# Performance work log

Hardware: AMD Instinct MI355X
Metric: run time of the kernel (lower is better)

Reference implementation:

```python
import jax, jax.numpy as jnp
import numpy as np

N, E, B = 20000, 320000, 16
DIN, HID, HEADS, ZDIM = 128, 128, 4, 128
NEG_SLOPE = 0.2


def _glorot(key, shape):
    fan = sum(shape[-2:]) if len(shape) >= 2 else shape[-1] * 2
    return jax.random.normal(key, shape, jnp.float32) * jnp.sqrt(2.0 / fan)


def setup_inputs() -> dict:
    key = jax.random.key(0)
    ks = jax.random.split(key, 20)
    inp = {
        "x": jax.random.normal(ks[0], (N, DIN), jnp.float32),
        "edge_index": jax.random.randint(ks[1], (2, E), 0, N),
        "batch_id": jnp.sort(jax.random.randint(ks[2], (N,), 0, B)),
        "node_mask": jax.random.bernoulli(ks[3], 0.1, (N,)),
        "edge_mask": jax.random.bernoulli(ks[4], 0.5, (E,)),
    }
    # layer dims: e_Fs=[128,128,128,128]; heads=4 on layers 0,1; heads=1 last
    dims = [(DIN, HID, HEADS), (HID * HEADS, HID, HEADS), (HID * HEADS, ZDIM, 1)]
    for li, (fin, fout, h) in enumerate(dims, start=1):
        inp[f"W{li}"] = _glorot(ks[4 + 3 * li], (fin, h * fout))
        inp[f"att_src{li}"] = _glorot(ks[5 + 3 * li], (h, fout))
        inp[f"att_dst{li}"] = _glorot(ks[6 + 3 * li], (h, fout))
        inp[f"bias{li}"] = jnp.zeros((h * fout,), jnp.float32)
    return inp


def _gat_layer(x, W, a_src, a_dst, bias, src, dst, heads, fout):
    n = x.shape[0]
    h = (x @ W).reshape(n, heads, fout)            # [N,H,F]
    alpha_s = (h * a_src).sum(-1)                  # [N,H]
    alpha_d = (h * a_dst).sum(-1)                  # [N,H]
    e = jax.nn.leaky_relu(alpha_s[src] + alpha_d[dst], NEG_SLOPE)  # [E,H]
    m = jax.ops.segment_max(e, dst, num_segments=n)
    ex = jnp.exp(e - m[dst])
    denom = jax.ops.segment_sum(ex, dst, num_segments=n)
    w = ex / denom[dst]                            # segment softmax over incoming edges
    out = jax.ops.segment_sum(h[src] * w[:, :, None], dst, num_segments=n)  # [N,H,F]
    return out.reshape(n, heads * fout) + bias


def reference(x, edge_index, batch_id, node_mask, edge_mask,
              W1, att_src1, att_dst1, bias1,
              W2, att_src2, att_dst2, bias2,
              W3, att_src3, att_dst3, bias3):
    n = x.shape[0]
    loop = jnp.arange(n)
    src = jnp.concatenate([edge_index[0], loop])   # add_self_loops=True
    dst = jnp.concatenate([edge_index[1], loop])
    # edge_mask is passed as edge_attr but GATConv has edge_dim=None -> ignored
    h = _gat_layer(x, W1, att_src1, att_dst1, bias1, src, dst, HEADS, HID)
    h = jax.nn.relu(h)
    h = _gat_layer(h, W2, att_src2, att_dst2, bias2, src, dst, HEADS, HID)
    h = jax.nn.relu(h)
    h = _gat_layer(h, W3, att_src3, att_dst3, bias3, src, dst, 1, ZDIM)
    # masked global max pool: if mask.sum()>0 pool over ~mask else all nodes
    has_masked = jnp.any(node_mask)
    valid = jnp.logical_or(~node_mask, ~has_masked)
    neg = jnp.asarray(-1e30, h.dtype)
    vals = jnp.where(valid[:, None], h, neg)
    return jax.ops.segment_max(vals, batch_id, num_segments=B)
```

## Files before the change

### kernel.cpp

```cpp
#include <hip/hip_runtime.h>
#include <stdint.h>


#define NN 20000
#define MPAD 20480
#define NE 320000
#define NBATCH 16
#define NEG 0.2f
#define WSCALE 64.0f
#define WINV 0.015625f

using f16x8 = __attribute__((ext_vector_type(8))) _Float16;
using f32x4 = __attribute__((ext_vector_type(4))) float;
using h2 = __attribute__((ext_vector_type(2))) _Float16;

#define GLL16(gp, lp)                                                        \
  __builtin_amdgcn_global_load_lds(                                          \
      (const __attribute__((address_space(1))) void*)(gp),                   \
      (__attribute__((address_space(3))) void*)(lp), 16, 0, 0)

static __device__ __forceinline__ unsigned short h2u(_Float16 h) {
  union { _Float16 f; unsigned short u; } c;
  c.f = h;
  return c.u;
}
static __device__ __forceinline__ float u2f(unsigned short u) {
  union { unsigned short u; _Float16 f; } c;
  c.u = u;
  return (float)c.f;
}
static __device__ __forceinline__ h2 bits2h2(unsigned v) {
  union { unsigned u; h2 h; } c;
  c.u = v;
  return c.h;
}
static __device__ __forceinline__ unsigned h22bits(h2 h) {
  union { h2 h; unsigned u; } c;
  c.h = h;
  return c.u;
}
static __device__ __forceinline__ unsigned encf(float f) {
  unsigned u = __float_as_uint(f);
  return (u & 0x80000000u) ? ~u : (u | 0x80000000u);
}
static __device__ __forceinline__ float decf(unsigned u) {
  return __uint_as_float((u & 0x80000000u) ? (u ^ 0x80000000u) : ~u);
}

#define R1 (512 * 128)
#define R2 (512 * 512)
#define R3 (128 * 512)
#define PREPTOT (R1 + R2 + R3 + NN * 128)
__global__ void k_init_prep(const float* __restrict__ W1, const float* __restrict__ W2,
                            const float* __restrict__ W3, const float* __restrict__ x,
                            unsigned short* __restrict__ wt1,
                            unsigned short* __restrict__ wt2,
                            unsigned short* __restrict__ wt3,
                            unsigned short* __restrict__ xp, int* deg,
                            unsigned* enc, int* flag, float* alz, int alcount) {
  int idx = blockIdx.x * blockDim.x + threadIdx.x;
  if (idx < R1) {
    int n = idx & 511, k = idx >> 9;
    wt1[(size_t)n * 128 + k] = h2u((_Float16)(W1[(size_t)k * 512 + n] * WSCALE));
  } else if (idx < R1 + R2) {
    int j = idx - R1;
    int n = j & 511, k = j >> 9;
    wt2[(size_t)n * 512 + k] = h2u((_Float16)(W2[(size_t)k * 512 + n] * WSCALE));
  } else if (idx < R1 + R2 + R3) {
    int j = idx - (R1 + R2);
    int n = j & 127, k = j >> 7;
    wt3[(size_t)n * 512 + k] = h2u((_Float16)(W3[(size_t)k * 128 + n] * WSCALE));
  } else if (idx < PREPTOT) {
    int j = idx - (R1 + R2 + R3);
    xp[j] = h2u((_Float16)x[j]);
  }
  if (idx < NN) deg[idx] = 1;
  if (idx < NBATCH * 128) enc[idx] = ~__float_as_uint(-1e30f);
  if (idx == 0) *flag = 0;
  if (idx < alcount) alz[idx] = 0.f;
}

__global__ void k_count(const int* __restrict__ ei, int* __restrict__ deg) {
  int e = blockIdx.x * blockDim.x + threadIdx.x;
  if (e < NE) atomicAdd(&deg[ei[NE + e]], 1);
}

__global__ void k_scan(const int* __restrict__ deg, int* __restrict__ row_ptr,
                       int* __restrict__ cursor) {
  __shared__ int wsum[16];
  int t = threadIdx.x;
  int lane = t & 63, wid = t >> 6;
  const int CH = 20;
  int beg = t * CH;
  int s = 0;
  for (int i = 0; i < CH; i++) {
    int idx = beg + i;
    if (idx < NN) s += deg[idx];
  }
  int incl = s;
  for (int off = 1; off < 64; off <<= 1) {
    int v = __shfl_up(incl, off, 64);
    if (lane >= off) incl += v;
  }
  if (lane == 63) wsum[wid] = incl;
  __syncthreads();
  if (t < 16) {
    int v = wsum[t];
    int in2 = v;
    for (int off = 1; off < 16; off <<= 1) {
      int u = __shfl_up(in2, off, 16);
      if (t >= off) in2 += u;
    }
    wsum[t] = in2 - v;
  }
  __syncthreads();
  int run = wsum[wid] + incl - s;
  for (int i = 0; i < CH; i++) {
    int idx = beg + i;
    if (idx < NN) {
      row_ptr[idx] = run;
      cursor[idx] = run;
      run += deg[idx];
    }
  }
  if (t == 1023) row_ptr[NN] = run;
}

__global__ void k_fill(const int* __restrict__ ei, int* __restrict__ cursor,
                       int* __restrict__ col, const int* __restrict__ nmask,
                       int* __restrict__ flag) {
  int i = blockIdx.x * blockDim.x + threadIdx.x;
  if (i >= NE + NN) return;
  int src, dst;
  if (i < NE) {
    src = ei[i];
    dst = ei[NE + i];
  } else {
    src = dst = i - NE;
    if (nmask[src] != 0) *flag = 1;
  }
  int pos = atomicAdd(&cursor[dst], 1);
  col[pos] = src;
}

#define BN 128
#define BK 32

template <int BMT, int NT, bool SWIZ>
__global__ __launch_bounds__(NT, 4) void k_gemm(
    const unsigned short* __restrict__ Ap, const unsigned short* __restrict__ Wt,
    unsigned short* __restrict__ C, const float* __restrict__ attS,
    const float* __restrict__ attD, float* __restrict__ alS,
    float* __restrict__ alD, int K, int Nc, int H) {
  __shared__ __align__(16) unsigned short As[BMT][BK];
  __shared__ __align__(16) unsigned short Bs[BN][BK];
  int tid = threadIdx.x;
  int bm, bn;
  if constexpr (SWIZ) {
    int id = blockIdx.x;
    int r = id & 7, t = id >> 3;
    bn = (t & 3) * BN;
    bm = (((t >> 2) << 3) + r) * BMT;
  } else {
    bm = blockIdx.y * BMT;
    bn = blockIdx.x * BN;
  }
  int wid = tid >> 6, lane = tid & 63;
  int wm = (BMT == 128) ? (wid >> 1) * 64 : 0;
  int wn = (BMT == 128) ? (wid & 1) * 64 : wid * 64;
  int lrow = lane & 15, lquad = lane >> 4;

  f32x4 acc[4][4] = {};

  for (int k0 = 0; k0 < K; k0 += BK) {
    __syncthreads();
#pragma unroll
    for (int i = 0; i < (BMT * 4) / NT; i++) {
      int slot = tid + NT * i;
      int row = slot >> 2;
      int ks = (slot & 3) * 8;
      GLL16(Ap + (size_t)(bm + row) * K + k0 + ks, &As[0][0] + (size_t)slot * 8);
    }
#pragma unroll
    for (int i = 0; i < 512 / NT; i++) {
      int slot = tid + NT * i;
      int row = slot >> 2;
      int ks = (slot & 3) * 8;
      GLL16(Wt + (size_t)(bn + row) * K + k0 + ks, &Bs[0][0] + (size_t)slot * 8);
    }
    __syncthreads();

    f16x8 af[4];
#pragma unroll
    for (int mf = 0; mf < 4; mf++)
      af[mf] = *(const f16x8*)&As[wm + mf * 16 + lrow][lquad * 8];
#pragma unroll
    for (int nf = 0; nf < 4; nf++) {
      f16x8 bf = *(const f16x8*)&Bs[wn + nf * 16 + lrow][lquad * 8];
#pragma unroll
      for (int mf = 0; mf < 4; mf++)
        acc[mf][nf] =
            __builtin_amdgcn_mfma_f32_16x16x32_f16(bf, af[mf], acc[mf][nf], 0, 0, 0);
    }
  }
#pragma unroll
  for (int mf = 0; mf < 4; mf++)
#pragma unroll
    for (int nf = 0; nf < 4; nf++)
#pragma unroll
      for (int r = 0; r < 4; r++) acc[mf][nf][r] *= WINV;

  float4 aS[4], aD[4];
#pragma unroll
  for (int nf = 0; nf < 4; nf++) {
    int n0 = bn + wn + nf * 16 + lquad * 4;
    aS[nf] = *(const float4*)(attS + n0);
    aD[nf] = *(const float4*)(attD + n0);
  }
  int head = bn >> 7;
#pragma unroll
  for (int mf = 0; mf < 4; mf++) {
    float ps = 0.f, pd = 0.f;
#pragma unroll
    for (int nf = 0; nf < 4; nf++) {
      ps += acc[mf][nf][0] * aS[nf].x + acc[mf][nf][1] * aS[nf].y +
            acc[mf][nf][2] * aS[nf].z + acc[mf][nf][3] * aS[nf].w;
      pd += acc[mf][nf][0] * aD[nf].x + acc[mf][nf][1] * aD[nf].y +
            acc[mf][nf][2] * aD[nf].z + acc[mf][nf][3] * aD[nf].w;
    }
    ps += __shfl_xor(ps, 16, 64);
    ps += __shfl_xor(ps, 32, 64);
    pd += __shfl_xor(pd, 16, 64);
    pd += __shfl_xor(pd, 32, 64);
    int row = bm + wm + mf * 16 + lrow;
    if (lquad == 0) {
      atomicAdd(&alS[(size_t)row * H + head], ps);
      atomicAdd(&alD[(size_t)row * H + head], pd);
    }
  }
#pragma unroll
  for (int mf = 0; mf < 4; mf++) {
    int m = bm + wm + mf * 16 + lrow;
#pragma unroll
    for (int nf = 0; nf < 4; nf++) {
      int n0 = bn + wn + nf * 16 + lquad * 4;
      ushort4 o;
      o.x = h2u((_Float16)acc[mf][nf][0]);
      o.y = h2u((_Float16)acc[mf][nf][1]);
      o.z = h2u((_Float16)acc[mf][nf][2]);
      o.w = h2u((_Float16)acc[mf][nf][3]);
      *(ushort4*)(C + (size_t)m * Nc + n0) = o;
    }
  }
}

template <int HF, int NG>
static __device__ __forceinline__ void gat_gather(
    const unsigned long long* __restrict__ cwp, int je, int se,
    const unsigned short* __restrict__ hb, h2& ha0, h2& ha1, h2& ha2, h2& ha3) {
  unsigned long long q[NG];
  uint4 v[NG];
#pragma unroll
  for (int r = 0; r < NG; r++) q[r] = cwp[je + se + 4 * r];
#pragma unroll
  for (int r = 0; r < NG; r++)
    v[r] = *(const uint4*)(hb + (size_t)(unsigned)q[r] * HF);
#pragma unroll
  for (int r = 0; r < NG; r++) {
    h2 hw = bits2h2((unsigned)(q[r] >> 32));
    ha0 += hw * bits2h2(v[r].x);
    ha1 += hw * bits2h2(v[r].y);
    ha2 += hw * bits2h2(v[r].z);
    ha3 += hw * bits2h2(v[r].w);
  }
}

template <int H, bool RELU, bool FP16OUT, bool PIN>
__global__ __launch_bounds__(256) void k_agg(
    const unsigned short* __restrict__ h, const float* __restrict__ as_,
    const float* __restrict__ ad_, const int* __restrict__ row_ptr,
    const int* __restrict__ col, const float* __restrict__ bias,
    float* __restrict__ out, unsigned short* __restrict__ outp) {
  constexpr int HF = H * 128;
  __shared__ unsigned long long cw[4][64];
  int tid = threadIdx.x, bwid = tid >> 6, lane = tid & 63;
  int node, sub;
  if constexpr (PIN) {
    sub = blockIdx.x & 3;
    node = (blockIdx.x >> 2) * 4 + bwid;
  } else {
    node = blockIdx.x * 4 + bwid;
    sub = 0;
    if (node >= NN) return;
  }
  int beg = row_ptr[node], end = row_ptr[node + 1];
  int deg = end - beg;
  float adv = ad_[(size_t)node * H + sub];
  float shift = (adv > 0.f) ? adv : NEG * adv;
  float fscale = 1.f;
  bool fast = (deg <= 64);

  if (__builtin_expect(fast, 1)) {
    unsigned sidx = 0;
    float t = 0.f;
    if (lane < deg) {
      sidx = (unsigned)col[beg + lane];
      float e = as_[(size_t)sidx * H + sub] + adv;
      e = (e > 0.f) ? e : NEG * e;
      t = fminf(__expf(e - shift), 60000.f);
    }
    _Float16 ht = (_Float16)t;
    h2 hv;
    hv[0] = ht;
    hv[1] = ht;
    cw[bwid][lane] = ((unsigned long long)h22bits(hv) << 32) | sidx;
    float S = t;
#pragma unroll
    for (int off = 32; off; off >>= 1) S += __shfl_xor(S, off, 64);
    fscale = 1.f / S;
  }
  float Mr = 0.f, Sinv = 0.f;
  if (!fast) {
    float m = -1e30f, s = 0.f;
    for (int j = beg + lane; j < end; j += 64) {
      int sidx = col[j];
      float e = as_[(size_t)sidx * H + sub] + adv;
      e = (e > 0.f) ? e : NEG * e;
      float nm = fmaxf(m, e);
      s = s * __expf(m - nm) + __expf(e - nm);
      m = nm;
    }
    float mm = m;
#pragma unroll
    for (int off = 32; off; off >>= 1) mm = fmaxf(mm, __shfl_xor(mm, off, 64));
    float t = s * __expf(m - mm);
#pragma unroll
    for (int off = 32; off; off >>= 1) t += __shfl_xor(t, off, 64);
    Mr = mm;
    Sinv = 1.f / t;
  }

  const int se = lane >> 4;
  const int fb = sub * 128 + (lane & 15) * 8;
  const unsigned short* __restrict__ hb = h + fb;
  float facc[8] = {0.f, 0.f, 0.f, 0.f, 0.f, 0.f, 0.f, 0.f};
  for (int c0 = beg; c0 < end; c0 += 64) {
    int cnt = min(64, end - c0);
    if (!fast) {
      unsigned sidx = 0;
      float w = 0.f;
      if (lane < cnt) {
        sidx = (unsigned)col[c0 + lane];
        float e = as_[(size_t)sidx * H + sub] + adv;
        e = (e > 0.f) ? e : NEG * e;
        w = __expf(e - Mr) * Sinv;
      }
      _Float16 hw = (_Float16)w;
      h2 hv;
      hv[0] = hw;
      hv[1] = hw;
      cw[bwid][lane] = ((unsigned long long)h22bits(hv) << 32) | sidx;
    }
    h2 ha0 = {(_Float16)0.f, (_Float16)0.f};
    h2 ha1 = ha0, ha2 = ha0, ha3 = ha0;
    int je = 0;
    while (je < cnt) {
      if (cnt - je > 16) {
        gat_gather<HF, 8>(cw[bwid], je, se, hb, ha0, ha1, ha2, ha3);
        je += 32;
      } else {
        gat_gather<HF, 4>(cw[bwid], je, se, hb, ha0, ha1, ha2, ha3);
        je += 16;
      }
    }
    facc[0] += (float)ha0[0];
    facc[1] += (float)ha0[1];
    facc[2] += (float)ha1[0];
    facc[3] += (float)ha1[1];
    facc[4] += (float)ha2[0];
    facc[5] += (float)ha2[1];
    facc[6] += (float)ha3[0];
    facc[7] += (float)ha3[1];
  }
#pragma unroll
  for (int k = 0; k < 8; k++) {
    facc[k] += __shfl_xor(facc[k], 16, 64);
    facc[k] += __shfl_xor(facc[k], 32, 64);
  }
  if (lane < 16) {
    float4 b0 = *(const float4*)(bias + fb);
    float4 b1 = *(const float4*)(bias + fb + 4);
    float v0 = facc[0] * fscale + b0.x, v1 = facc[1] * fscale + b0.y;
    float v2 = facc[2] * fscale + b0.z, v3 = facc[3] * fscale + b0.w;
    float v4 = facc[4] * fscale + b1.x, v5 = facc[5] * fscale + b1.y;
    float v6 = facc[6] * fscale + b1.z, v7 = facc[7] * fscale + b1.w;
    if (RELU) {
      v0 = fmaxf(v0, 0.f);
      v1 = fmaxf(v1, 0.f);
      v2 = fmaxf(v2, 0.f);
      v3 = fmaxf(v3, 0.f);
      v4 = fmaxf(v4, 0.f);
      v5 = fmaxf(v5, 0.f);
      v6 = fmaxf(v6, 0.f);
      v7 = fmaxf(v7, 0.f);
    }
    if constexpr (FP16OUT) {
      h2 p0, p1, p2, p3;
      p0[0] = (_Float16)v0;
      p0[1] = (_Float16)v1;
      p1[0] = (_Float16)v2;
      p1[1] = (_Float16)v3;
      p2[0] = (_Float16)v4;
      p2[1] = (_Float16)v5;
      p3[0] = (_Float16)v6;
      p3[1] = (_Float16)v7;
      uint4 o;
      o.x = h22bits(p0);
      o.y = h22bits(p1);
      o.z = h22bits(p2);
      o.w = h22bits(p3);
      *(uint4*)(outp + (size_t)node * HF + fb) = o;
    } else {
      *(float4*)(out + (size_t)node * HF + fb) = make_float4(v0, v1, v2, v3);
      *(float4*)(out + (size_t)node * HF + fb + 4) = make_float4(v4, v5, v6, v7);
    }
  }
}

__global__ void k_pool(const unsigned short* __restrict__ h,
                       const int* __restrict__ batch,
                       const int* __restrict__ mask, const int* __restrict__ flag,
                       unsigned* __restrict__ enc) {
  int f = threadIdx.x;
  int n0 = blockIdx.x * 32;
  if (n0 >= NN) return;
  int n1 = min(NN, n0 + 32);
  int any = *flag;
  float local = -1e30f;
  int curb = batch[n0];
  for (int n = n0; n < n1; ++n) {
    int b = batch[n];
    if (b != curb) {
      if (local > -1e30f) atomicMax(&enc[curb * 128 + f], encf(local));
      local = -1e30f;
      curb = b;
    }
    bool valid = (mask[n] == 0) || (!any);
    if (valid) local = fmaxf(local, u2f(h[(size_t)n * 128 + f]));
  }
  if (local > -1e30f) atomicMax(&enc[curb * 128 + f], encf(local));
}

__global__ void k_out(const unsigned* __restrict__ enc, float* __restrict__ out) {
  int i = blockIdx.x * blockDim.x + threadIdx.x;
  if (i < NBATCH * 128) out[i] = decf(enc[i]);
}

extern "C" void kernel_launch(void* const* d_in, const int* in_sizes, int n_in,
                              void* d_out, int out_size, void* d_ws, size_t ws_size,
                              hipStream_t stream) {
  const float* x = (const float*)d_in[0];
  const int* ei = (const int*)d_in[1];
  const int* batch = (const int*)d_in[2];
  const int* nmask = (const int*)d_in[3];
  const float* W1 = (const float*)d_in[5];
  const float* as1 = (const float*)d_in[6];
  const float* ad1 = (const float*)d_in[7];
  const float* b1 = (const float*)d_in[8];
  const float* W2 = (const float*)d_in[9];
  const float* as2 = (const float*)d_in[10];
  const float* ad2 = (const float*)d_in[11];
  const float* b2 = (const float*)d_in[12];
  const float* W3 = (const float*)d_in[13];
  const float* as3 = (const float*)d_in[14];
  const float* ad3 = (const float*)d_in[15];
  const float* b3 = (const float*)d_in[16];

  char* ws = (char*)d_ws;
  size_t off = 0;
  auto alloc = [&](size_t bytes) -> char* {
    char* p = ws + off;
    off = (off + bytes + 255) & ~(size_t)255;
    return p;
  };
  unsigned short* hA = (unsigned short*)alloc((size_t)MPAD * 512 * 2);
  unsigned short* hG = (unsigned short*)alloc((size_t)MPAD * 512 * 2);
  float* out3 = (float*)alloc((size_t)MPAD * 128 * 4);
  unsigned short* xP = (unsigned short*)out3;
  unsigned short* out3h = (unsigned short*)out3;
  unsigned short* wt1 = (unsigned short*)alloc((size_t)512 * 128 * 2);
  unsigned short* wt2 = (unsigned short*)alloc((size_t)512 * 512 * 2);
  unsigned short* wt3 = (unsigned short*)alloc((size_t)128 * 512 * 2);
  char* alStart = ws + off;
  float* alS1 = (float*)alloc((size_t)MPAD * 4 * 4);
  float* alD1 = (float*)alloc((size_t)MPAD * 4 * 4);
  float* alS2 = (float*)alloc((size_t)MPAD * 4 * 4);
  float* alD2 = (float*)alloc((size_t)MPAD * 4 * 4);
  float* alS3 = (float*)alloc((size_t)MPAD * 4);
  float* alD3 = (float*)alloc((size_t)MPAD * 4);
  int alcount = (int)(((ws + off) - alStart) / 4);
  int* deg = (int*)alloc((size_t)NN * 4);
  int* cursor = (int*)alloc((size_t)NN * 4);
  int* rowp = (int*)alloc((size_t)(NN + 1) * 4);
  int* colx = (int*)alloc((size_t)(NE + NN) * 4);
  unsigned* enc = (unsigned*)alloc((size_t)NBATCH * 128 * 4);
  int* flag = (int*)alloc(4);
  (void)ws_size; (void)n_in; (void)in_sizes; (void)out_size;

  k_init_prep<<<(PREPTOT + 255) / 256, 256, 0, stream>>>(
      W1, W2, W3, x, wt1, wt2, wt3, xP, deg, enc, flag, (float*)alStart, alcount);
  k_count<<<(NE + 255) / 256, 256, 0, stream>>>(ei, deg);
  k_scan<<<1, 1024, 0, stream>>>(deg, rowp, cursor);
  k_fill<<<(NE + NN + 255) / 256, 256, 0, stream>>>(ei, cursor, colx, nmask, flag);

  const int gemmBlocks = 4 * (MPAD / 128);
  dim3 gg3(1, MPAD / 64);

  k_gemm<128, 256, true><<<gemmBlocks, 256, 0, stream>>>(
      xP, wt1, hA, as1, ad1, alS1, alD1, 128, 512, 4);
  k_agg<4, true, true, true><<<NN, 256, 0, stream>>>(hA, alS1, alD1, rowp, colx,
                                                     b1, nullptr, hG);
  k_gemm<128, 256, true><<<gemmBlocks, 256, 0, stream>>>(
      hG, wt2, hA, as2, ad2, alS2, alD2, 512, 512, 4);
  k_agg<4, true, true, true><<<NN, 256, 0, stream>>>(hA, alS2, alD2, rowp, colx,
                                                     b2, nullptr, hG);
  k_gemm<64, 128, false><<<gg3, 128, 0, stream>>>(hG, wt3, hA, as3, ad3, alS3,
                                                  alD3, 512, 128, 1);
  k_agg<1, false, true, false><<<(NN + 3) / 4, 256, 0, stream>>>(
      hA, alS3, alD3, rowp, colx, b3, nullptr, out3h);

  k_pool<<<(NN + 31) / 32, 128, 0, stream>>>(out3h, batch, nmask, flag, enc);
  k_out<<<(NBATCH * 128 + 255) / 256, 256, 0, stream>>>(enc, (float*)d_out);
}
```

Measured before the change: 326.9 us.

## Process two destination nodes per wavefront in GAT aggregation

Each 64-lane wavefront now handles two destination nodes with 32 lanes each, where before one wavefront handled one node. The shared edge-weight buffer is split per half-wave, and softmax reductions use 32-lane shuffles. The gather loop steps over 16 or 8 edges using the larger degree of the pair. The aim is to cut idle lanes and block count, since average degree is around 17 and most of a 64-lane wave sat unused. In exchange, the pair shares the larger node's trip count, and nodes with more than 32 edges now take the slow path.

```diff
diff --git a/kernel.cpp b/kernel.cpp
--- a/kernel.cpp
+++ b/kernel.cpp
@@ -261,7 +261,7 @@
   unsigned long long q[NG];
   uint4 v[NG];
 #pragma unroll
-  for (int r = 0; r < NG; r++) q[r] = cwp[je + se + 4 * r];
+  for (int r = 0; r < NG; r++) q[r] = cwp[je + se + 2 * r];
 #pragma unroll
   for (int r = 0; r < NG; r++)
     v[r] = *(const uint4*)(hb + (size_t)(unsigned)q[r] * HF);
@@ -282,29 +282,31 @@
     const int* __restrict__ col, const float* __restrict__ bias,
     float* __restrict__ out, unsigned short* __restrict__ outp) {
   constexpr int HF = H * 128;
-  __shared__ unsigned long long cw[4][64];
+  __shared__ unsigned long long cw[4][2][32];
   int tid = threadIdx.x, bwid = tid >> 6, lane = tid & 63;
+  int ns = lane >> 5, sl = lane & 31;
   int node, sub;
   if constexpr (PIN) {
     sub = blockIdx.x & 3;
-    node = (blockIdx.x >> 2) * 4 + bwid;
+    node = (blockIdx.x >> 2) * 8 + bwid * 2 + ns;
   } else {
-    node = blockIdx.x * 4 + bwid;
+    node = blockIdx.x * 8 + bwid * 2 + ns;
     sub = 0;
-    if (node >= NN) return;
-  }
+  }
+  if (node >= NN) node = NN - 1;
   int beg = row_ptr[node], end = row_ptr[node + 1];
   int deg = end - beg;
+  int degmax = max(deg, __shfl_xor(deg, 32, 64));
+  bool fast = (degmax <= 32);
   float adv = ad_[(size_t)node * H + sub];
   float shift = (adv > 0.f) ? adv : NEG * adv;
   float fscale = 1.f;
-  bool fast = (deg <= 64);
 
   if (__builtin_expect(fast, 1)) {
     unsigned sidx = 0;
     float t = 0.f;
-    if (lane < deg) {
-      sidx = (unsigned)col[beg + lane];
+    if (sl < deg) {
+      sidx = (unsigned)col[beg + sl];
       float e = as_[(size_t)sidx * H + sub] + adv;
       e = (e > 0.f) ? e : NEG * e;
       t = fminf(__expf(e - shift), 60000.f);
@@ -313,16 +315,16 @@
     h2 hv;
     hv[0] = ht;
     hv[1] = ht;
-    cw[bwid][lane] = ((unsigned long long)h22bits(hv) << 32) | sidx;
+    cw[bwid][ns][sl] = ((unsigned long long)h22bits(hv) << 32) | sidx;
     float S = t;
 #pragma unroll
-    for (int off = 32; off; off >>= 1) S += __shfl_xor(S, off, 64);
+    for (int off = 16; off; off >>= 1) S += __shfl_xor(S, off, 64);
     fscale = 1.f / S;
   }
   float Mr = 0.f, Sinv = 0.f;
   if (!fast) {
     float m = -1e30f, s = 0.f;
-    for (int j = beg + lane; j < end; j += 64) {
+    for (int j = beg + sl; j < end; j += 32) {
       int sidx = col[j];
       float e = as_[(size_t)sidx * H + sub] + adv;
       e = (e > 0.f) ? e : NEG * e;
@@ -332,25 +334,28 @@
     }
     float mm = m;
 #pragma unroll
-    for (int off = 32; off; off >>= 1) mm = fmaxf(mm, __shfl_xor(mm, off, 64));
+    for (int off = 16; off; off >>= 1) mm = fmaxf(mm, __shfl_xor(mm, off, 64));
     float t = s * __expf(m - mm);
 #pragma unroll
-    for (int off = 32; off; off >>= 1) t += __shfl_xor(t, off, 64);
+    for (int off = 16; off; off >>= 1) t += __shfl_xor(t, off, 64);
     Mr = mm;
     Sinv = 1.f / t;
   }
 
-  const int se = lane >> 4;
+  const int se = (lane >> 4) & 1;
   const int fb = sub * 128 + (lane & 15) * 8;
   const unsigned short* __restrict__ hb = h + fb;
   float facc[8] = {0.f, 0.f, 0.f, 0.f, 0.f, 0.f, 0.f, 0.f};
-  for (int c0 = beg; c0 < end; c0 += 64) {
-    int cnt = min(64, end - c0);
+  int nchunk = fast ? 1 : ((degmax + 31) >> 5);
+  for (int ch = 0; ch < nchunk; ch++) {
+    int c0 = beg + ch * 32;
+    int cnt = end - c0;
+    cnt = (cnt > 32) ? 32 : cnt;
     if (!fast) {
       unsigned sidx = 0;
       float w = 0.f;
-      if (lane < cnt) {
-        sidx = (unsigned)col[c0 + lane];
+      if (sl < cnt) {
+        sidx = (unsigned)col[c0 + sl];
         float e = as_[(size_t)sidx * H + sub] + adv;
         e = (e > 0.f) ? e : NEG * e;
         w = __expf(e - Mr) * Sinv;
@@ -359,18 +364,20 @@
       h2 hv;
       hv[0] = hw;
       hv[1] = hw;
-      cw[bwid][lane] = ((unsigned long long)h22bits(hv) << 32) | sidx;
-    }
+      cw[bwid][ns][sl] = ((unsigned long long)h22bits(hv) << 32) | sidx;
+    }
+    int cntu = fast ? degmax : max(cnt, __shfl_xor(cnt, 32, 64));
     h2 ha0 = {(_Float16)0.f, (_Float16)0.f};
     h2 ha1 = ha0, ha2 = ha0, ha3 = ha0;
+    const unsigned long long* cwp = cw[bwid][ns];
     int je = 0;
-    while (je < cnt) {
-      if (cnt - je > 16) {
-        gat_gather<HF, 8>(cw[bwid], je, se, hb, ha0, ha1, ha2, ha3);
-        je += 32;
+    while (je < cntu) {
+      if (cntu - je > 8) {
+        gat_gather<HF, 8>(cwp, je, se, hb, ha0, ha1, ha2, ha3);
+        je += 16;
       } else {
-        gat_gather<HF, 4>(cw[bwid], je, se, hb, ha0, ha1, ha2, ha3);
-        je += 16;
+        gat_gather<HF, 4>(cwp, je, se, hb, ha0, ha1, ha2, ha3);
+        je += 8;
       }
     }
     facc[0] += (float)ha0[0];
@@ -383,11 +390,8 @@
     facc[7] += (float)ha3[1];
   }
 #pragma unroll
-  for (int k = 0; k < 8; k++) {
-    facc[k] += __shfl_xor(facc[k], 16, 64);
-    facc[k] += __shfl_xor(facc[k], 32, 64);
-  }
-  if (lane < 16) {
+  for (int k = 0; k < 8; k++) facc[k] += __shfl_xor(facc[k], 16, 64);
+  if (sl < 16) {
     float4 b0 = *(const float4*)(bias + fb);
     float4 b1 = *(const float4*)(bias + fb + 4);
     float v0 = facc[0] * fscale + b0.x, v1 = facc[1] * fscale + b0.y;
@@ -515,18 +519,20 @@
 
   const int gemmBlocks = 4 * (MPAD / 128);
   dim3 gg3(1, MPAD / 64);
+  const int aggBlocks = NN / 2;
+  const int aggBlocks3 = NN / 8;
 
   k_gemm<128, 256, true><<<gemmBlocks, 256, 0, stream>>>(
       xP, wt1, hA, as1, ad1, alS1, alD1, 128, 512, 4);
-  k_agg<4, true, true, true><<<NN, 256, 0, stream>>>(hA, alS1, alD1, rowp, colx,
-                                                     b1, nullptr, hG);
+  k_agg<4, true, true, true><<<aggBlocks, 256, 0, stream>>>(
+      hA, alS1, alD1, rowp, colx, b1, nullptr, hG);
   k_gemm<128, 256, true><<<gemmBlocks, 256, 0, stream>>>(
       hG, wt2, hA, as2, ad2, alS2, alD2, 512, 512, 4);
-  k_agg<4, true, true, true><<<NN, 256, 0, stream>>>(hA, alS2, alD2, rowp, colx,
-                                                     b2, nullptr, hG);
+  k_agg<4, true, true, true><<<aggBlocks, 256, 0, stream>>>(
+      hA, alS2, alD2, rowp, colx, b2, nullptr, hG);
   k_gemm<64, 128, false><<<gg3, 128, 0, stream>>>(hG, wt3, hA, as3, ad3, alS3,
                                                   alD3, 512, 128, 1);
-  k_agg<1, false, true, false><<<(NN + 3) / 4, 256, 0, stream>>>(
+  k_agg<1, false, true, false><<<aggBlocks3, 256, 0, stream>>>(
       hA, alS3, alD3, rowp, colx, b3, nullptr, out3h);
 
   k_pool<<<(NN + 31) / 32, 128, 0, stream>>>(out3h, batch, nmask, flag, enc);
```

Result: faster. 314.6 us, median of 2 (-3.8%).
